# Kernel tuning notes

Hardware: AMD Instinct MI355X
Metric: run time of the kernel (lower is better)

Reference implementation:

```python
import jax, jax.numpy as jnp
import numpy as np
import math

H = 1e-4  # finite-difference step
TW = math.pi / 8.0  # transition width
LOW = math.pi / 2.0 - TW
HIGH = math.pi / 2.0 + TW


def _smooth_step(t):
    # equivalent to torch smooth_step with masks: 0 below LOW, 1 above HIGH,
    x = jnp.clip((t - LOW) / (HIGH - LOW), 0.0, 1.0)
    return x * x * (3.0 - 2.0 * x)


def _compute_potential(xyz, a_param, b_param, direction):
    # xyz: [B,3]
    a = jnp.clip(a_param, 0.0, 20.0)
    b = jnp.clip(b_param, 0.0, 20.0)
    r2 = jnp.sum(xyz * xyz, axis=1)          # [B]
    r = jnp.sqrt(r2)
    origin = r == 0.0
    safe_r = jnp.where(origin, 1.0, r)
    p_hat = xyz / safe_r[:, None]            # [B,3]
    dot = p_hat @ direction                  # [B]
    theta = jnp.arccos(jnp.clip(dot, -1.0, 1.0))
    w = _smooth_step(theta)
    # w*direct + (1-w)*ray = 0.5*a*r^2 + (1-w)*0.5*b*r^2*theta^2
    pot = 0.5 * a * r2 + (1.0 - w) * 0.5 * b * r2 * theta * theta
    return jnp.where(origin, 0.0, pot)


def setup_inputs() -> dict:
    key = jax.random.key(0)
    B = 8388608
    xyz = jax.random.normal(key, (B, 3), dtype=jnp.float32)
    theta_dir, phi_dir = 1.0471975511965976, 0.7853981633974483
    direction = jnp.array([
        math.sin(theta_dir) * math.cos(phi_dir),
        math.sin(theta_dir) * math.sin(phi_dir),
        math.cos(theta_dir),
    ], dtype=jnp.float32)
    a_param = jnp.float32(1.0)
    b_param = jnp.float32(10.0)
    return {"xyz": xyz, "a_param": a_param, "b_param": b_param, "direction": direction}


def reference(xyz, a_param, b_param, direction):
    # compute_velocity: central finite differences of the potential, negated
    eye = jnp.eye(3, dtype=xyz.dtype)
    grads = []
    for i in range(3):  # fixed tiny loop over xyz axes
        u_plus = _compute_potential(xyz + H * eye[i], a_param, b_param, direction)
        u_minus = _compute_potential(xyz - H * eye[i], a_param, b_param, direction)
        grads.append((u_plus - u_minus) / (2.0 * H))
    velocity = -jnp.stack(grads, axis=1)  # [B,3]
    return velocity
```

## Files before the change

### kernel.cpp

```cpp
#include <hip/hip_runtime.h>
#include <math.h>

#define LOW_F   1.1780972450961724f
#define INV_TW  1.2732395447351628f
#define WP_K    7.639437268410977f

__device__ __forceinline__ float fast_acos(float x) {
    float s = __builtin_fabsf(x);
    bool big = s > 0.5f;
    float z = big ? fmaf(-0.5f, s, 0.5f) : x * x;
    float r = big ? __builtin_amdgcn_sqrtf(z) : s;
    float p = fmaf(z, 4.2163199048e-2f, 2.4181311049e-2f);
    p = fmaf(z, p, 4.5470025998e-2f);
    p = fmaf(z, p, 7.4953002686e-2f);
    p = fmaf(z, p, 1.6666752422e-1f);
    float asn = fmaf(r * z, p, r);
    float t2 = 2.0f * asn;
    float rb = (x >= 0.0f) ? t2 : (3.14159274f - t2);
    float rs = (x >= 0.0f) ? (1.57079637f - asn) : (1.57079637f + asn);
    return big ? rb : rs;
}

__device__ __forceinline__ void point_velocity(float x, float y, float z,
                                               float a, float b,
                                               float dx, float dy, float dz,
                                               float& vx, float& vy, float& vz) {
    float r2 = x * x + y * y + z * z;
    float r = __builtin_amdgcn_sqrtf(r2);
    float invr = __builtin_amdgcn_rcpf(r);
    float dot = (x * dx + y * dy + z * dz) * invr;
    dot = fminf(fmaxf(dot, -1.0f), 1.0f);
    float theta = fast_acos(dot);

    float t = (theta - LOW_F) * INV_TW;
    t = fminf(fmaxf(t, 0.0f), 1.0f);
    float w = t * t * (3.0f - 2.0f * t);
    float one_m_w = 1.0f - w;
    float wp = WP_K * t * (1.0f - t);

    float th2 = theta * theta;
    float k1 = fmaf(b * th2, one_m_w, a);

    float sin2 = fmaf(-dot, dot, 1.0f);
    float sinth = __builtin_amdgcn_sqrtf(fmaxf(sin2, 0.0f));
    float rcpsin = __builtin_amdgcn_rcpf(fmaxf(sinth, 1e-30f));
    float num = fmaf(2.0f * theta, one_m_w, -th2 * wp);
    float k2 = (r * 0.5f * b) * num * rcpsin;

    float m = dot * invr;
    float gx = fmaf(-m, x, dx);
    float gy = fmaf(-m, y, dy);
    float gz = fmaf(-m, z, dz);

    float ovx = fmaf(-k1, x, k2 * gx);
    float ovy = fmaf(-k1, y, k2 * gy);
    float ovz = fmaf(-k1, z, k2 * gz);

    bool origin = (r2 == 0.0f);
    vx = origin ? 0.0f : ovx;
    vy = origin ? 0.0f : ovy;
    vz = origin ? 0.0f : ovz;
}

extern "C" __global__ void __launch_bounds__(256)
canyon3d_grad_kernel(const float* __restrict__ xyz,
                     const float* __restrict__ a_param,
                     const float* __restrict__ b_param,
                     const float* __restrict__ dir,
                     float* __restrict__ out,
                     int B) {
    int t = blockIdx.x * blockDim.x + threadIdx.x;
    int base = t * 4;
    if (base >= B) return;

    float a = fminf(fmaxf(a_param[0], 0.0f), 20.0f);
    float b = fminf(fmaxf(b_param[0], 0.0f), 20.0f);
    float dx = dir[0], dy = dir[1], dz = dir[2];

    if (base + 4 <= B) {
        const float4* in4 = (const float4*)xyz;
        float4 A  = in4[3 * t + 0];
        float4 Bv = in4[3 * t + 1];
        float4 C  = in4[3 * t + 2];

        float o0, o1, o2, o3, o4, o5, o6, o7, o8, o9, o10, o11;
        point_velocity(A.x, A.y, A.z,   a, b, dx, dy, dz, o0, o1, o2);
        point_velocity(A.w, Bv.x, Bv.y, a, b, dx, dy, dz, o3, o4, o5);
        point_velocity(Bv.z, Bv.w, C.x, a, b, dx, dy, dz, o6, o7, o8);
        point_velocity(C.y, C.z, C.w,   a, b, dx, dy, dz, o9, o10, o11);

        float4* out4 = (float4*)out;
        out4[3 * t + 0] = make_float4(o0, o1, o2, o3);
        out4[3 * t + 1] = make_float4(o4, o5, o6, o7);
        out4[3 * t + 2] = make_float4(o8, o9, o10, o11);
    } else {
        for (int i = base; i < B; ++i) {
            float x = xyz[3 * i], y = xyz[3 * i + 1], z = xyz[3 * i + 2];
            float vx, vy, vz;
            point_velocity(x, y, z, a, b, dx, dy, dz, vx, vy, vz);
            out[3 * i] = vx; out[3 * i + 1] = vy; out[3 * i + 2] = vz;
        }
    }
}

extern "C" void kernel_launch(void* const* d_in, const int* in_sizes, int n_in,
                              void* d_out, int out_size, void* d_ws, size_t ws_size,
                              hipStream_t stream) {
    const float* xyz = (const float*)d_in[0];
    const float* a_param = (const float*)d_in[1];
    const float* b_param = (const float*)d_in[2];
    const float* dir = (const float*)d_in[3];
    float* out = (float*)d_out;

    int B = in_sizes[0] / 3;
    int nthreads = (B + 3) / 4;
    dim3 block(256);
    dim3 grid((nthreads + 255) / 256);
    canyon3d_grad_kernel<<<grid, block, 0, stream>>>(xyz, a_param, b_param, dir, out, B);
}
```

Before: 184.8 us.

## Use grid-stride loop with software-prefetched loads and nontemporal stores

Replaces the one-quad-per-thread launch with a fixed grid of 2048 blocks that walks the data in a grid-stride loop. Each iteration loads the next quad of points before computing the current one, and writes outputs with nontemporal stores to limit cache pollution. The aim is to overlap memory latency with compute and cut block launch overhead on this streaming kernel. In exchange, fewer waves are resident, the prefetch buffer raises register pressure, and the tail points are handled separately.

```diff
diff --git a/kernel.cpp b/kernel.cpp
--- a/kernel.cpp
+++ b/kernel.cpp
@@ -4,6 +4,8 @@
 #define LOW_F   1.1780972450961724f
 #define INV_TW  1.2732395447351628f
 #define WP_K    7.639437268410977f
+
+typedef float floatx4 __attribute__((ext_vector_type(4)));
 
 __device__ __forceinline__ float fast_acos(float x) {
     float s = __builtin_fabsf(x);
@@ -69,37 +71,58 @@
                      const float* __restrict__ dir,
                      float* __restrict__ out,
                      int B) {
-    int t = blockIdx.x * blockDim.x + threadIdx.x;
-    int base = t * 4;
-    if (base >= B) return;
+    int nquad = B >> 2;
+    int tid = blockIdx.x * blockDim.x + threadIdx.x;
+    int stride = gridDim.x * blockDim.x;
 
     float a = fminf(fmaxf(a_param[0], 0.0f), 20.0f);
     float b = fminf(fmaxf(b_param[0], 0.0f), 20.0f);
     float dx = dir[0], dy = dir[1], dz = dir[2];
 
-    if (base + 4 <= B) {
-        const float4* in4 = (const float4*)xyz;
-        float4 A  = in4[3 * t + 0];
-        float4 Bv = in4[3 * t + 1];
-        float4 C  = in4[3 * t + 2];
+    const floatx4* in4 = (const floatx4*)xyz;
+    floatx4* out4 = (floatx4*)out;
 
-        float o0, o1, o2, o3, o4, o5, o6, o7, o8, o9, o10, o11;
-        point_velocity(A.x, A.y, A.z,   a, b, dx, dy, dz, o0, o1, o2);
-        point_velocity(A.w, Bv.x, Bv.y, a, b, dx, dy, dz, o3, o4, o5);
-        point_velocity(Bv.z, Bv.w, C.x, a, b, dx, dy, dz, o6, o7, o8);
-        point_velocity(C.y, C.z, C.w,   a, b, dx, dy, dz, o9, o10, o11);
+    int q = tid;
+    if (q < nquad) {
+        floatx4 A  = in4[3 * q + 0];
+        floatx4 Bv = in4[3 * q + 1];
+        floatx4 C  = in4[3 * q + 2];
+        for (;;) {
+            int qn = q + stride;
+            bool more = qn < nquad;
+            floatx4 An, Bn, Cn;
+            if (more) {
+                An = in4[3 * qn + 0];
+                Bn = in4[3 * qn + 1];
+                Cn = in4[3 * qn + 2];
+            }
 
-        float4* out4 = (float4*)out;
-        out4[3 * t + 0] = make_float4(o0, o1, o2, o3);
-        out4[3 * t + 1] = make_float4(o4, o5, o6, o7);
-        out4[3 * t + 2] = make_float4(o8, o9, o10, o11);
-    } else {
-        for (int i = base; i < B; ++i) {
-            float x = xyz[3 * i], y = xyz[3 * i + 1], z = xyz[3 * i + 2];
-            float vx, vy, vz;
-            point_velocity(x, y, z, a, b, dx, dy, dz, vx, vy, vz);
-            out[3 * i] = vx; out[3 * i + 1] = vy; out[3 * i + 2] = vz;
+            float o0, o1, o2, o3, o4, o5, o6, o7, o8, o9, o10, o11;
+            point_velocity(A.x, A.y, A.z,   a, b, dx, dy, dz, o0, o1, o2);
+            point_velocity(A.w, Bv.x, Bv.y, a, b, dx, dy, dz, o3, o4, o5);
+            point_velocity(Bv.z, Bv.w, C.x, a, b, dx, dy, dz, o6, o7, o8);
+            point_velocity(C.y, C.z, C.w,   a, b, dx, dy, dz, o9, o10, o11);
+
+            floatx4 O0 = {o0, o1, o2, o3};
+            floatx4 O1 = {o4, o5, o6, o7};
+            floatx4 O2 = {o8, o9, o10, o11};
+            __builtin_nontemporal_store(O0, &out4[3 * q + 0]);
+            __builtin_nontemporal_store(O1, &out4[3 * q + 1]);
+            __builtin_nontemporal_store(O2, &out4[3 * q + 2]);
+
+            if (!more) break;
+            q = qn; A = An; Bv = Bn; C = Cn;
         }
+    }
+
+    int done = nquad << 2;
+    int rem = B - done;
+    if (tid < rem) {
+        int i = done + tid;
+        float x = xyz[3 * i], y = xyz[3 * i + 1], z = xyz[3 * i + 2];
+        float vx, vy, vz;
+        point_velocity(x, y, z, a, b, dx, dy, dz, vx, vy, vz);
+        out[3 * i] = vx; out[3 * i + 1] = vy; out[3 * i + 2] = vz;
     }
 }
 
@@ -113,8 +136,9 @@
     float* out = (float*)d_out;
 
     int B = in_sizes[0] / 3;
-    int nthreads = (B + 3) / 4;
-    dim3 block(256);
-    dim3 grid((nthreads + 255) / 256);
-    canyon3d_grad_kernel<<<grid, block, 0, stream>>>(xyz, a_param, b_param, dir, out, B);
+    int nquad = B / 4;
+    int blocks = 2048;
+    int maxBlocks = (nquad + 255) / 256;
+    if (blocks > maxBlocks) blocks = maxBlocks > 0 ? maxBlocks : 1;
+    canyon3d_grad_kernel<<<dim3(blocks), dim3(256), 0, stream>>>(xyz, a_param, b_param, dir, out, B);
 }
```

New measurement: 204.3 us. +10.6%, slower.
